# Kernel optimization log

Hardware: AMD Instinct MI355X
Metric: run time of the kernel (lower is better)

## Reference

```python
import jax, jax.numpy as jnp
import numpy as np

HEADS = 4

def _proj(x, w, b):
    # 1x1 conv == per-pixel linear: x [B,C,H,W], w [O,C], b [O]
    return jnp.einsum('oc,bchw->bohw', w, x) + b[None, :, None, None]

def setup_inputs() -> dict:
    key = jax.random.key(0)
    ks = jax.random.split(key, 9)
    B, C, H, W = 16, 512, 32, 32
    emb = C // HEADS
    return {
        'x': jax.random.normal(ks[0], (B, C, H, W), jnp.float32),
        'wq_w': jax.random.normal(ks[1], (C, C), jnp.float32) * 0.02,
        'wq_b': jax.random.normal(ks[2], (C,), jnp.float32) * 0.02,
        'wk_w': jax.random.normal(ks[3], (C, C), jnp.float32) * 0.02,
        'wk_b': jax.random.normal(ks[4], (C,), jnp.float32) * 0.02,
        'wv_w': jax.random.normal(ks[5], (C, C), jnp.float32) * 0.02,
        'wv_b': jax.random.normal(ks[6], (C,), jnp.float32) * 0.02,
        'rh': jax.random.normal(ks[7], (1, HEADS, emb, 1, H), jnp.float32),
        'rw': jax.random.normal(ks[8], (1, HEADS, emb, W, 1), jnp.float32),
    }

def reference(x, wq_w, wq_b, wk_w, wk_b, wv_w, wv_b, rh, rw):
    B, C, H, W = x.shape
    heads = HEADS
    emb = C // heads
    scale = C ** (-0.5)
    N = H * W
    q = _proj(x, wq_w, wq_b).reshape(B, heads, emb, N).transpose(0, 1, 3, 2) * scale  # [B,h,N,d]
    kt = _proj(x, wk_w, wk_b).reshape(B, heads, emb, N)                               # [B,h,d,N]
    v = _proj(x, wv_w, wv_b).reshape(B, heads, emb, N).transpose(0, 1, 3, 2)          # [B,h,N,d]
    qkt = jnp.matmul(q, kt)                                                           # [B,h,N,N]
    # relative-position term: (rh + rw) broadcasts to [1,h,d,W,H], flattened as in source
    rt = (rh + rw).reshape(1, heads, emb, N)
    qrt = jnp.matmul(q, rt)                                                           # [B,h,N,N]
    attn = jax.nn.softmax(qkt + qrt, axis=-1)
    y = jnp.matmul(attn, v)                                                           # [B,h,N,d]
    return y.reshape(B, C, H, W)
```

## Files before the change

### kernel.cpp

```cpp
#include <hip/hip_runtime.h>
#include <hip/hip_bf16.h>
#include <cstdint>

#define NB 16
#define NC 512
#define NPIX 1024
#define NHEADS 4
#define NEMB 128

typedef short bf16x8 __attribute__((ext_vector_type(8)));
typedef float f32x4 __attribute__((ext_vector_type(4)));
typedef float f32x16 __attribute__((ext_vector_type(16)));
typedef unsigned short u16x4 __attribute__((ext_vector_type(4)));
typedef unsigned short u16x8 __attribute__((ext_vector_type(8)));

__device__ __forceinline__ unsigned short f2bf(float f) {
  union { float f; unsigned u; } c; c.f = f;
  return (unsigned short)((c.u + 0x7FFFu + ((c.u >> 16) & 1u)) >> 16);
}

__device__ __forceinline__ unsigned cvtpk_bf16(float lo, float hi) {
  unsigned r;
  asm("v_cvt_pk_bf16_f32 %0, %1, %2" : "=v"(r) : "v"(lo), "v"(hi));
  return r;
}

__device__ __forceinline__ void gload_lds16(const void* g, void* l) {
  __builtin_amdgcn_global_load_lds(
      (const __attribute__((address_space(1))) unsigned int*)g,
      (__attribute__((address_space(3))) unsigned int*)l, 16, 0, 0);
}

__global__ void k_prep_x(const float* __restrict__ x, unsigned short* __restrict__ xt) {
  __shared__ float tile[4][32][33];
  int bid = blockIdx.x;
  int nt = bid & 31, ct4 = (bid >> 5) & 3, b = bid >> 7;
  int n0 = nt * 32, c0 = ct4 * 128;
  int t = threadIdx.x;
  int r = t >> 3, q = t & 7;
#pragma unroll
  for (int s = 0; s < 4; s++) {
    float4 v = *(const float4*)(x + ((size_t)(b * NC + c0 + s * 32 + r)) * NPIX + n0 + q * 4);
    tile[s][r][q * 4 + 0] = v.x; tile[s][r][q * 4 + 1] = v.y;
    tile[s][r][q * 4 + 2] = v.z; tile[s][r][q * 4 + 3] = v.w;
  }
  __syncthreads();
  int cl = q * 4;
#pragma unroll
  for (int s = 0; s < 4; s++) {
    u16x4 o;
    o[0] = f2bf(tile[s][cl + 0][r]); o[1] = f2bf(tile[s][cl + 1][r]);
    o[2] = f2bf(tile[s][cl + 2][r]); o[3] = f2bf(tile[s][cl + 3][r]);
    *(u16x4*)(xt + ((size_t)(b * NPIX + n0 + r)) * NC + c0 + s * 32 + cl) = o;
  }
}

__global__ void k_prep_w(const float* __restrict__ wq, const float* __restrict__ wk,
                         const float* __restrict__ wv, unsigned short* __restrict__ wb) {
  const float* src = blockIdx.y == 0 ? wq : (blockIdx.y == 1 ? wk : wv);
  unsigned short* dst = wb + (size_t)blockIdx.y * NC * NC;
  for (int i = blockIdx.x * 256 + threadIdx.x; i < NC * NC / 4; i += gridDim.x * 256) {
    float4 v = ((const float4*)src)[i];
    u16x4 o = { f2bf(v.x), f2bf(v.y), f2bf(v.z), f2bf(v.w) };
    ((u16x4*)dst)[i] = o;
  }
}

__global__ __launch_bounds__(256, 3) void k_qkv(
    const unsigned short* __restrict__ wb, const unsigned short* __restrict__ xt,
    const float* __restrict__ qb, const float* __restrict__ kb, const float* __restrict__ vb,
    const float* __restrict__ rh, const float* __restrict__ rw,
    unsigned short* __restrict__ Qs, unsigned short* __restrict__ Kn,
    unsigned short* __restrict__ Vm) {
  __shared__ unsigned short Alds[128 * 64];
  __shared__ unsigned short Blds[128 * 64];
  int bid = blockIdx.x;
  int nt = bid & 7, mt = (bid >> 3) & 3;
  int rest = bid >> 5;
  int p = rest % 3, b = rest / 3;
  int m0 = mt * 128, n0 = nt * 128;
  const unsigned short* A = wb + (size_t)p * NC * NC + (size_t)m0 * NC;
  const unsigned short* Bx = xt + (size_t)b * NPIX * NC + (size_t)n0 * NC;
  int t = threadIdx.x;
  int lane = t & 63, wid = t >> 6;
  int wm = (wid >> 1) * 64, wn = (wid & 1) * 64;
  f32x4 acc[4][4] = {};
  for (int k0 = 0; k0 < NC; k0 += 64) {
#pragma unroll
    for (int i = 0; i < 4; i++) {
      int idx = i * 256 + t;
      int row = idx >> 3, col = (idx & 7) * 8;
      gload_lds16(A + (size_t)row * NC + k0 + col, &Alds[idx * 8]);
    }
#pragma unroll
    for (int i = 0; i < 4; i++) {
      int idx = i * 256 + t;
      int row = idx >> 3, col = (idx & 7) * 8;
      gload_lds16(Bx + (size_t)row * NC + k0 + col, &Blds[idx * 8]);
    }
    __syncthreads();
#pragma unroll
    for (int ks = 0; ks < 2; ks++) {
      int kk = ks * 32 + ((lane >> 4) << 3);
      bf16x8 af[4], bfr[4];
#pragma unroll
      for (int f = 0; f < 4; f++)
        af[f] = *(const bf16x8*)&Alds[(wm + f * 16 + (lane & 15)) * 64 + kk];
#pragma unroll
      for (int f = 0; f < 4; f++)
        bfr[f] = *(const bf16x8*)&Blds[(wn + f * 16 + (lane & 15)) * 64 + kk];
#pragma unroll
      for (int fm = 0; fm < 4; fm++)
#pragma unroll
        for (int fn = 0; fn < 4; fn++)
          acc[fm][fn] = __builtin_amdgcn_mfma_f32_16x16x32_bf16(af[fm], bfr[fn], acc[fm][fn], 0, 0, 0);
    }
    __syncthreads();
  }
  const float scale = 0.044194173824159216f * 1.4426950408889634f;
  if (p == 2) {
    char* vbase = (char*)(Vm + (size_t)(b * NHEADS + mt) * 16 * 8192);
#pragma unroll
    for (int fm = 0; fm < 4; fm++) {
#pragma unroll
      for (int r = 0; r < 4; r++) {
        int d = wm + fm * 16 + ((lane >> 4) << 2) + r;
        float bv = vb[m0 + d];
        char* vt = vbase + (size_t)d * 128;
#pragma unroll
        for (int fn = 0; fn < 4; fn++) {
          int j = n0 + wn + fn * 16 + (lane & 15);
          int tile = j >> 6, jl = j & 63;
          *(unsigned short*)(vt + tile * 16384 + (((jl * 2)) ^ ((d & 7) << 4))) =
              f2bf(acc[fm][fn][r] + bv);
        }
      }
    }
  } else if (p == 1) {
    char* kbase = (char*)(Kn + (size_t)(b * NHEADS + mt) * 16 * 8192);
#pragma unroll
    for (int fm = 0; fm < 4; fm++) {
      int e0 = wm + fm * 16 + ((lane >> 4) << 2);
#pragma unroll
      for (int fn = 0; fn < 4; fn++) {
        int j = n0 + wn + fn * 16 + (lane & 15);
        int tile = j >> 6, jl = j & 63;
        u16x4 o;
#pragma unroll
        for (int r = 0; r < 4; r++) {
          float v = acc[fm][fn][r] + kb[m0 + e0 + r];
          v += rh[(m0 + e0 + r) * 32 + (j & 31)] + rw[(m0 + e0 + r) * 32 + (j >> 5)];
          o[r] = f2bf(v);
        }
        *(u16x4*)(kbase + tile * 16384 + jl * 256 + ((2 * e0) ^ ((jl & 7) << 4))) = o;
      }
    }
  } else {
    unsigned short* dst = Qs + ((size_t)((b * NHEADS + mt) * NPIX + n0)) * NEMB;
#pragma unroll
    for (int fm = 0; fm < 4; fm++) {
      int e0 = wm + fm * 16 + ((lane >> 4) << 2);
#pragma unroll
      for (int fn = 0; fn < 4; fn++) {
        int ncol = wn + fn * 16 + (lane & 15);
        u16x4 o;
#pragma unroll
        for (int r = 0; r < 4; r++)
          o[r] = f2bf((acc[fm][fn][r] + qb[m0 + e0 + r]) * scale);
        *(u16x4*)&dst[(size_t)ncol * NEMB + e0] = o;
      }
    }
  }
}

__global__ __launch_bounds__(256, 2) void k_attn(
    const unsigned short* __restrict__ Qs, const unsigned short* __restrict__ Kp,
    const unsigned short* __restrict__ Vp, float* __restrict__ out) {
  __shared__ __align__(16) char smem[65536];
  int bid = blockIdx.x;
  int pair = bid & 63;
  int b = pair >> 2, hd = pair & 3;
  int i0 = (bid >> 6) * 128;
  int t = threadIdx.x, w = t >> 6, lane = t & 63;
  int l31 = lane & 31, hi5 = lane >> 5;
  const unsigned short* Qb = Qs + (size_t)pair * NPIX * NEMB;
  const char* Kpb = (const char*)(Kp + (size_t)pair * 16 * 8192);
  const char* Vpb = (const char*)(Vp + (size_t)pair * 16 * 8192);

  bf16x8 qf[8];
  {
    const unsigned short* qr = Qb + (size_t)(i0 + w * 32 + l31) * NEMB + hi5 * 8;
#pragma unroll
    for (int d8 = 0; d8 < 8; d8++) qf[d8] = *(const bf16x8*)(qr + d8 * 16);
  }
  f32x16 yacc[4] = {};
  float l = 0.f;

#pragma unroll
  for (int r = 0; r < 4; r++) {
    gload_lds16(Kpb + r * 4096 + t * 16, smem + r * 4096 + t * 16);
    gload_lds16(Vpb + r * 4096 + t * 16, smem + 32768 + r * 4096 + t * 16);
  }
  __syncthreads();

  for (int tt = 0; tt < 16; tt++) {
    int cur = tt & 1;
    if (tt < 15) {
      const char* kn = Kpb + (tt + 1) * 16384;
      const char* vn = Vpb + (tt + 1) * 16384;
      char* kd = smem + (cur ^ 1) * 16384;
      char* vd = smem + 32768 + (cur ^ 1) * 16384;
#pragma unroll
      for (int r = 0; r < 4; r++) {
        gload_lds16(kn + r * 4096 + t * 16, kd + r * 4096 + t * 16);
        gload_lds16(vn + r * 4096 + t * 16, vd + r * 4096 + t * 16);
      }
    }
    const char* Kl = smem + cur * 16384;
    const char* Vl = smem + 32768 + cur * 16384;
    f32x16 sacc[2] = {};
    {
      int swz = (l31 & 7) << 4;
#pragma unroll
      for (int d8 = 0; d8 < 8; d8++) {
        int colb = (d8 * 32 + hi5 * 16) ^ swz;
        bf16x8 k0 = *(const bf16x8*)(Kl + l31 * 256 + colb);
        bf16x8 k1 = *(const bf16x8*)(Kl + (32 + l31) * 256 + colb);
        __builtin_amdgcn_s_setprio(1);
        sacc[0] = __builtin_amdgcn_mfma_f32_32x32x16_bf16(k0, qf[d8], sacc[0], 0, 0, 0);
        sacc[1] = __builtin_amdgcn_mfma_f32_32x32x16_bf16(k1, qf[d8], sacc[1], 0, 0, 0);
        __builtin_amdgcn_s_setprio(0);
      }
    }
    float rs0 = 0.f, rs1 = 0.f, rs2 = 0.f, rs3 = 0.f;
#pragma unroll
    for (int c = 0; c < 2; c++)
#pragma unroll
      for (int i = 0; i < 16; i += 4) {
        float p0 = exp2f(sacc[c][i + 0]);
        float p1 = exp2f(sacc[c][i + 1]);
        float p2 = exp2f(sacc[c][i + 2]);
        float p3 = exp2f(sacc[c][i + 3]);
        sacc[c][i + 0] = p0; sacc[c][i + 1] = p1;
        sacc[c][i + 2] = p2; sacc[c][i + 3] = p3;
        rs0 += p0; rs1 += p1; rs2 += p2; rs3 += p3;
      }
    l += (rs0 + rs1) + (rs2 + rs3);
    unsigned up[2][4][2];
#pragma unroll
    for (int c = 0; c < 2; c++)
#pragma unroll
      for (int g = 0; g < 4; g++) {
        up[c][g][0] = cvtpk_bf16(sacc[c][4 * g + 0], sacc[c][4 * g + 1]);
        up[c][g][1] = cvtpk_bf16(sacc[c][4 * g + 2], sacc[c][4 * g + 3]);
      }
    bf16x8 pf[4];
#pragma unroll
    for (int c2 = 0; c2 < 4; c2++) {
      int c = c2 >> 1, gA = (c2 & 1) * 2, gB = gA + 1;
      unsigned a0 = up[c][gA][0], b0 = up[c][gB][0];
      unsigned a1 = up[c][gA][1], b1 = up[c][gB][1];
      asm("v_permlane32_swap_b32 %0, %1" : "+v"(a0), "+v"(b0));
      asm("v_permlane32_swap_b32 %0, %1" : "+v"(a1), "+v"(b1));
      unsigned wd[4] = { a0, a1, b0, b1 };
      pf[c2] = *(bf16x8*)wd;
    }
    {
      int swz = (l31 & 7) << 4;
#pragma unroll
      for (int c2 = 0; c2 < 4; c2++) {
        int colb = (c2 * 32 + hi5 * 16) ^ swz;
        __builtin_amdgcn_s_setprio(1);
#pragma unroll
        for (int ds = 0; ds < 4; ds++) {
          bf16x8 vf = *(const bf16x8*)(Vl + (ds * 32 + l31) * 128 + colb);
          yacc[ds] = __builtin_amdgcn_mfma_f32_32x32x16_bf16(vf, pf[c2], yacc[ds], 0, 0, 0);
        }
        __builtin_amdgcn_s_setprio(0);
      }
    }
    __syncthreads();
  }
  float ltot = l + __shfl_xor(l, 32);
  float invl = 1.0f / ltot;
  int q = i0 + w * 32 + l31;
  float* orow = out + ((size_t)(b * NC + hd * NEMB + (q >> 3))) * NPIX + (q & 7) * NEMB;
#pragma unroll
  for (int ds = 0; ds < 4; ds++)
#pragma unroll
    for (int rg = 0; rg < 4; rg++) {
      f32x4 v;
#pragma unroll
      for (int i = 0; i < 4; i++) v[i] = yacc[ds][rg * 4 + i] * invl;
      *(f32x4*)(orow + ds * 32 + rg * 8 + hi5 * 4) = v;
    }
}

extern "C" void kernel_launch(void* const* d_in, const int* in_sizes, int n_in,
                              void* d_out, int out_size, void* d_ws, size_t ws_size,
                              hipStream_t stream) {
  const float* x  = (const float*)d_in[0];
  const float* wq = (const float*)d_in[1];
  const float* qb = (const float*)d_in[2];
  const float* wk = (const float*)d_in[3];
  const float* kb = (const float*)d_in[4];
  const float* wv = (const float*)d_in[5];
  const float* vb = (const float*)d_in[6];
  const float* rh = (const float*)d_in[7];
  const float* rw = (const float*)d_in[8];
  float* out = (float*)d_out;
  char* ws = (char*)d_ws;
  unsigned short* xt = (unsigned short*)(ws);
  unsigned short* wb = (unsigned short*)(ws + 16777216);
  unsigned short* Q  = (unsigned short*)(ws + 18350080);
  unsigned short* K  = (unsigned short*)(ws + 35127296);
  unsigned short* V  = (unsigned short*)(ws + 51904512);
  k_prep_x<<<2048, 256, 0, stream>>>(x, xt);
  k_prep_w<<<dim3(64, 3), 256, 0, stream>>>(wq, wk, wv, wb);
  k_qkv<<<1536, 256, 0, stream>>>(wb, xt, qb, kb, vb, rh, rw, Q, K, V);
  k_attn<<<512, 256, 0, stream>>>(Q, K, V, out);
}
```

Before: 103.6 us.

## Load K/V fragments directly from global memory in MFMA-ready layout, drop LDS staging

The projection kernel now writes K and V in a fragment-major layout, so each lane's 16-byte MFMA operand sits contiguously in global memory. The attention kernel drops the double-buffered LDS staging and its barriers and reads K/V fragments straight from global (and L2) into registers each tile. This removes LDS traffic and block-wide synchronisation. In exchange, each of the four waves re-reads the same K/V from cache, raising global/L2 load volume, register pressure from holding 32 fragment registers, and exposing load latency without explicit prefetch.

```diff
diff --git a/kernel.cpp b/kernel.cpp
--- a/kernel.cpp
+++ b/kernel.cpp
@@ -119,28 +119,29 @@
   }
   const float scale = 0.044194173824159216f * 1.4426950408889634f;
   if (p == 2) {
-    char* vbase = (char*)(Vm + (size_t)(b * NHEADS + mt) * 16 * 8192);
+    unsigned short* vbase = Vm + (size_t)(b * NHEADS + mt) * 131072;
 #pragma unroll
     for (int fm = 0; fm < 4; fm++) {
 #pragma unroll
       for (int r = 0; r < 4; r++) {
         int d = wm + fm * 16 + ((lane >> 4) << 2) + r;
         float bv = vb[m0 + d];
-        char* vt = vbase + (size_t)d * 128;
 #pragma unroll
         for (int fn = 0; fn < 4; fn++) {
           int j = n0 + wn + fn * 16 + (lane & 15);
           int tile = j >> 6, jl = j & 63;
-          *(unsigned short*)(vt + tile * 16384 + (((jl * 2)) ^ ((d & 7) << 4))) =
-              f2bf(acc[fm][fn][r] + bv);
+          int c2 = jl >> 4, h5 = (jl >> 3) & 1, j8 = jl & 7;
+          size_t flat = ((((size_t)tile * 4 + c2) * 2 + h5) * 128 + d) * 8 + j8;
+          vbase[flat] = f2bf(acc[fm][fn][r] + bv);
         }
       }
     }
   } else if (p == 1) {
-    char* kbase = (char*)(Kn + (size_t)(b * NHEADS + mt) * 16 * 8192);
+    unsigned short* kbase = Kn + (size_t)(b * NHEADS + mt) * 131072;
 #pragma unroll
     for (int fm = 0; fm < 4; fm++) {
       int e0 = wm + fm * 16 + ((lane >> 4) << 2);
+      int d8 = e0 >> 4, h5 = (e0 >> 3) & 1, e8 = e0 & 7;
 #pragma unroll
       for (int fn = 0; fn < 4; fn++) {
         int j = n0 + wn + fn * 16 + (lane & 15);
@@ -152,7 +153,8 @@
           v += rh[(m0 + e0 + r) * 32 + (j & 31)] + rw[(m0 + e0 + r) * 32 + (j >> 5)];
           o[r] = f2bf(v);
         }
-        *(u16x4*)(kbase + tile * 16384 + jl * 256 + ((2 * e0) ^ ((jl & 7) << 4))) = o;
+        size_t flat = ((((size_t)tile * 8 + d8) * 2 + h5) * 64 + jl) * 8 + e8;
+        *(u16x4*)(kbase + flat) = o;
       }
     }
   } else {
@@ -176,7 +178,6 @@
 __global__ __launch_bounds__(256, 2) void k_attn(
     const unsigned short* __restrict__ Qs, const unsigned short* __restrict__ Kp,
     const unsigned short* __restrict__ Vp, float* __restrict__ out) {
-  __shared__ __align__(16) char smem[65536];
   int bid = blockIdx.x;
   int pair = bid & 63;
   int b = pair >> 2, hd = pair & 3;
@@ -184,8 +185,8 @@
   int t = threadIdx.x, w = t >> 6, lane = t & 63;
   int l31 = lane & 31, hi5 = lane >> 5;
   const unsigned short* Qb = Qs + (size_t)pair * NPIX * NEMB;
-  const char* Kpb = (const char*)(Kp + (size_t)pair * 16 * 8192);
-  const char* Vpb = (const char*)(Vp + (size_t)pair * 16 * 8192);
+  const unsigned short* Kg = Kp + (size_t)pair * 131072;
+  const unsigned short* Vg = Vp + (size_t)pair * 131072;
 
   bf16x8 qf[8];
   {
@@ -196,42 +197,29 @@
   f32x16 yacc[4] = {};
   float l = 0.f;
 
-#pragma unroll
-  for (int r = 0; r < 4; r++) {
-    gload_lds16(Kpb + r * 4096 + t * 16, smem + r * 4096 + t * 16);
-    gload_lds16(Vpb + r * 4096 + t * 16, smem + 32768 + r * 4096 + t * 16);
-  }
-  __syncthreads();
-
   for (int tt = 0; tt < 16; tt++) {
-    int cur = tt & 1;
-    if (tt < 15) {
-      const char* kn = Kpb + (tt + 1) * 16384;
-      const char* vn = Vpb + (tt + 1) * 16384;
-      char* kd = smem + (cur ^ 1) * 16384;
-      char* vd = smem + 32768 + (cur ^ 1) * 16384;
-#pragma unroll
-      for (int r = 0; r < 4; r++) {
-        gload_lds16(kn + r * 4096 + t * 16, kd + r * 4096 + t * 16);
-        gload_lds16(vn + r * 4096 + t * 16, vd + r * 4096 + t * 16);
-      }
-    }
-    const char* Kl = smem + cur * 16384;
-    const char* Vl = smem + 32768 + cur * 16384;
+    bf16x8 kf0[8], kf1[8];
+#pragma unroll
+    for (int d8 = 0; d8 < 8; d8++) {
+      const unsigned short* kp = Kg + (((size_t)tt * 8 + d8) * 2 + hi5) * 512;
+      kf0[d8] = *(const bf16x8*)(kp + l31 * 8);
+      kf1[d8] = *(const bf16x8*)(kp + (l31 + 32) * 8);
+    }
     f32x16 sacc[2] = {};
-    {
-      int swz = (l31 & 7) << 4;
-#pragma unroll
-      for (int d8 = 0; d8 < 8; d8++) {
-        int colb = (d8 * 32 + hi5 * 16) ^ swz;
-        bf16x8 k0 = *(const bf16x8*)(Kl + l31 * 256 + colb);
-        bf16x8 k1 = *(const bf16x8*)(Kl + (32 + l31) * 256 + colb);
-        __builtin_amdgcn_s_setprio(1);
-        sacc[0] = __builtin_amdgcn_mfma_f32_32x32x16_bf16(k0, qf[d8], sacc[0], 0, 0, 0);
-        sacc[1] = __builtin_amdgcn_mfma_f32_32x32x16_bf16(k1, qf[d8], sacc[1], 0, 0, 0);
-        __builtin_amdgcn_s_setprio(0);
-      }
-    }
+    __builtin_amdgcn_s_setprio(1);
+#pragma unroll
+    for (int d8 = 0; d8 < 8; d8++) {
+      sacc[0] = __builtin_amdgcn_mfma_f32_32x32x16_bf16(kf0[d8], qf[d8], sacc[0], 0, 0, 0);
+      sacc[1] = __builtin_amdgcn_mfma_f32_32x32x16_bf16(kf1[d8], qf[d8], sacc[1], 0, 0, 0);
+    }
+    __builtin_amdgcn_s_setprio(0);
+    bf16x8 vf[4][4];
+#pragma unroll
+    for (int c2 = 0; c2 < 4; c2++)
+#pragma unroll
+      for (int ds = 0; ds < 4; ds++)
+        vf[c2][ds] = *(const bf16x8*)(
+            Vg + ((((size_t)tt * 4 + c2) * 2 + hi5) * 128 + ds * 32 + l31) * 8);
     float rs0 = 0.f, rs1 = 0.f, rs2 = 0.f, rs3 = 0.f;
 #pragma unroll
     for (int c = 0; c < 2; c++)
@@ -265,21 +253,13 @@
       unsigned wd[4] = { a0, a1, b0, b1 };
       pf[c2] = *(bf16x8*)wd;
     }
-    {
-      int swz = (l31 & 7) << 4;
-#pragma unroll
-      for (int c2 = 0; c2 < 4; c2++) {
-        int colb = (c2 * 32 + hi5 * 16) ^ swz;
-        __builtin_amdgcn_s_setprio(1);
-#pragma unroll
-        for (int ds = 0; ds < 4; ds++) {
-          bf16x8 vf = *(const bf16x8*)(Vl + (ds * 32 + l31) * 128 + colb);
-          yacc[ds] = __builtin_amdgcn_mfma_f32_32x32x16_bf16(vf, pf[c2], yacc[ds], 0, 0, 0);
-        }
-        __builtin_amdgcn_s_setprio(0);
-      }
-    }
-    __syncthreads();
+    __builtin_amdgcn_s_setprio(1);
+#pragma unroll
+    for (int c2 = 0; c2 < 4; c2++)
+#pragma unroll
+      for (int ds = 0; ds < 4; ds++)
+        yacc[ds] = __builtin_amdgcn_mfma_f32_32x32x16_bf16(vf[c2][ds], pf[c2], yacc[ds], 0, 0, 0);
+    __builtin_amdgcn_s_setprio(0);
   }
   float ltot = l + __shfl_xor(l, 32);
   float invl = 1.0f / ltot;
```

Result: slower. 107.6 us (+3.9%).

## Split attention key range across two wave groups per block and merge

Applied to the files above, without the earlier changes.

The attention kernel now launches 512 threads per block. Two halves of the block each process half of every 64-key tile (32 keys) for the same 128 queries, and their partial outputs and row sums are merged through shared memory at the end. The K and V workspace layouts in the projection kernel are changed to 32-key sub-tiles with new swizzles so each half reads its own contiguous region. This aims to raise the number of waves in flight and hide latency. The cost is an extra reduction pass through LDS and a slightly larger shared-memory footprint.

```diff
diff --git a/kernel.cpp b/kernel.cpp
--- a/kernel.cpp
+++ b/kernel.cpp
@@ -119,32 +119,30 @@
   }
   const float scale = 0.044194173824159216f * 1.4426950408889634f;
   if (p == 2) {
-    char* vbase = (char*)(Vm + (size_t)(b * NHEADS + mt) * 16 * 8192);
+    char* vbase = (char*)(Vm + (size_t)(b * NHEADS + mt) * 131072);
 #pragma unroll
     for (int fm = 0; fm < 4; fm++) {
 #pragma unroll
       for (int r = 0; r < 4; r++) {
         int d = wm + fm * 16 + ((lane >> 4) << 2) + r;
         float bv = vb[m0 + d];
-        char* vt = vbase + (size_t)d * 128;
 #pragma unroll
         for (int fn = 0; fn < 4; fn++) {
           int j = n0 + wn + fn * 16 + (lane & 15);
-          int tile = j >> 6, jl = j & 63;
-          *(unsigned short*)(vt + tile * 16384 + (((jl * 2)) ^ ((d & 7) << 4))) =
+          *(unsigned short*)(vbase + (size_t)(j >> 5) * 8192 + d * 64 +
+                             (((j & 31) * 2) ^ ((d & 3) << 4))) =
               f2bf(acc[fm][fn][r] + bv);
         }
       }
     }
   } else if (p == 1) {
-    char* kbase = (char*)(Kn + (size_t)(b * NHEADS + mt) * 16 * 8192);
+    char* kbase = (char*)(Kn + (size_t)(b * NHEADS + mt) * 131072);
 #pragma unroll
     for (int fm = 0; fm < 4; fm++) {
       int e0 = wm + fm * 16 + ((lane >> 4) << 2);
 #pragma unroll
       for (int fn = 0; fn < 4; fn++) {
         int j = n0 + wn + fn * 16 + (lane & 15);
-        int tile = j >> 6, jl = j & 63;
         u16x4 o;
 #pragma unroll
         for (int r = 0; r < 4; r++) {
@@ -152,7 +150,7 @@
           v += rh[(m0 + e0 + r) * 32 + (j & 31)] + rw[(m0 + e0 + r) * 32 + (j >> 5)];
           o[r] = f2bf(v);
         }
-        *(u16x4*)(kbase + tile * 16384 + jl * 256 + ((2 * e0) ^ ((jl & 7) << 4))) = o;
+        *(u16x4*)(kbase + (size_t)j * 256 + ((2 * e0) ^ ((j & 15) << 4))) = o;
       }
     }
   } else {
@@ -173,127 +171,136 @@
   }
 }
 
-__global__ __launch_bounds__(256, 2) void k_attn(
+__global__ __launch_bounds__(512, 4) void k_attn(
     const unsigned short* __restrict__ Qs, const unsigned short* __restrict__ Kp,
     const unsigned short* __restrict__ Vp, float* __restrict__ out) {
-  __shared__ __align__(16) char smem[65536];
+  __shared__ __align__(16) char smem[68096];
   int bid = blockIdx.x;
   int pair = bid & 63;
   int b = pair >> 2, hd = pair & 3;
   int i0 = (bid >> 6) * 128;
   int t = threadIdx.x, w = t >> 6, lane = t & 63;
   int l31 = lane & 31, hi5 = lane >> 5;
+  int h = w >> 2, wq = w & 3;
   const unsigned short* Qb = Qs + (size_t)pair * NPIX * NEMB;
-  const char* Kpb = (const char*)(Kp + (size_t)pair * 16 * 8192);
-  const char* Vpb = (const char*)(Vp + (size_t)pair * 16 * 8192);
+  const char* Kpb = (const char*)(Kp + (size_t)pair * 131072);
+  const char* Vpb = (const char*)(Vp + (size_t)pair * 131072);
 
   bf16x8 qf[8];
   {
-    const unsigned short* qr = Qb + (size_t)(i0 + w * 32 + l31) * NEMB + hi5 * 8;
+    const unsigned short* qr = Qb + (size_t)(i0 + wq * 32 + l31) * NEMB + hi5 * 8;
 #pragma unroll
     for (int d8 = 0; d8 < 8; d8++) qf[d8] = *(const bf16x8*)(qr + d8 * 16);
   }
   f32x16 yacc[4] = {};
   float l = 0.f;
 
-#pragma unroll
-  for (int r = 0; r < 4; r++) {
-    gload_lds16(Kpb + r * 4096 + t * 16, smem + r * 4096 + t * 16);
-    gload_lds16(Vpb + r * 4096 + t * 16, smem + 32768 + r * 4096 + t * 16);
-  }
+  auto stage = [&](int tile, int slot) {
+    char* kd = smem + slot * 16384;
+    char* vd = smem + 32768 + slot * 16384;
+#pragma unroll
+    for (int ii = 0; ii < 2; ii++) {
+      const char* ks = Kpb + (size_t)((ii * 16 + tile) * 8192) + t * 16;
+      const char* vs = Vpb + (size_t)((ii * 16 + tile) * 8192) + t * 16;
+      gload_lds16(ks, kd + (ii * 512 + t) * 16);
+      gload_lds16(vs, vd + (ii * 512 + t) * 16);
+    }
+  };
+
+  stage(0, 0);
   __syncthreads();
+
+  const int kswz = (l31 & 15) << 4;
+  const int vswz = (l31 & 3) << 4;
 
   for (int tt = 0; tt < 16; tt++) {
     int cur = tt & 1;
-    if (tt < 15) {
-      const char* kn = Kpb + (tt + 1) * 16384;
-      const char* vn = Vpb + (tt + 1) * 16384;
-      char* kd = smem + (cur ^ 1) * 16384;
-      char* vd = smem + 32768 + (cur ^ 1) * 16384;
-#pragma unroll
-      for (int r = 0; r < 4; r++) {
-        gload_lds16(kn + r * 4096 + t * 16, kd + r * 4096 + t * 16);
-        gload_lds16(vn + r * 4096 + t * 16, vd + r * 4096 + t * 16);
-      }
-    }
-    const char* Kl = smem + cur * 16384;
-    const char* Vl = smem + 32768 + cur * 16384;
-    f32x16 sacc[2] = {};
+    if (tt < 15) stage(tt + 1, cur ^ 1);
+    const char* Kl = smem + cur * 16384 + h * 8192;
+    const char* Vl = smem + 32768 + cur * 16384 + h * 8192;
+    f32x16 sacc = (f32x16)(0.0f);
+    __builtin_amdgcn_s_setprio(1);
+#pragma unroll
+    for (int d8 = 0; d8 < 8; d8++) {
+      bf16x8 k0 = *(const bf16x8*)(Kl + l31 * 256 + ((d8 * 32 + hi5 * 16) ^ kswz));
+      sacc = __builtin_amdgcn_mfma_f32_32x32x16_bf16(k0, qf[d8], sacc, 0, 0, 0);
+    }
+    __builtin_amdgcn_s_setprio(0);
+    float rs0, rs1, rs2, rs3;
     {
-      int swz = (l31 & 7) << 4;
-#pragma unroll
-      for (int d8 = 0; d8 < 8; d8++) {
-        int colb = (d8 * 32 + hi5 * 16) ^ swz;
-        bf16x8 k0 = *(const bf16x8*)(Kl + l31 * 256 + colb);
-        bf16x8 k1 = *(const bf16x8*)(Kl + (32 + l31) * 256 + colb);
-        __builtin_amdgcn_s_setprio(1);
-        sacc[0] = __builtin_amdgcn_mfma_f32_32x32x16_bf16(k0, qf[d8], sacc[0], 0, 0, 0);
-        sacc[1] = __builtin_amdgcn_mfma_f32_32x32x16_bf16(k1, qf[d8], sacc[1], 0, 0, 0);
-        __builtin_amdgcn_s_setprio(0);
-      }
-    }
-    float rs0 = 0.f, rs1 = 0.f, rs2 = 0.f, rs3 = 0.f;
-#pragma unroll
-    for (int c = 0; c < 2; c++)
-#pragma unroll
-      for (int i = 0; i < 16; i += 4) {
-        float p0 = exp2f(sacc[c][i + 0]);
-        float p1 = exp2f(sacc[c][i + 1]);
-        float p2 = exp2f(sacc[c][i + 2]);
-        float p3 = exp2f(sacc[c][i + 3]);
-        sacc[c][i + 0] = p0; sacc[c][i + 1] = p1;
-        sacc[c][i + 2] = p2; sacc[c][i + 3] = p3;
-        rs0 += p0; rs1 += p1; rs2 += p2; rs3 += p3;
-      }
+      float p0 = exp2f(sacc[0]), p1 = exp2f(sacc[1]), p2 = exp2f(sacc[2]), p3 = exp2f(sacc[3]);
+      sacc[0] = p0; sacc[1] = p1; sacc[2] = p2; sacc[3] = p3;
+      rs0 = p0; rs1 = p1; rs2 = p2; rs3 = p3;
+    }
+#pragma unroll
+    for (int i = 4; i < 16; i += 4) {
+      float p0 = exp2f(sacc[i + 0]);
+      float p1 = exp2f(sacc[i + 1]);
+      float p2 = exp2f(sacc[i + 2]);
+      float p3 = exp2f(sacc[i + 3]);
+      sacc[i + 0] = p0; sacc[i + 1] = p1; sacc[i + 2] = p2; sacc[i + 3] = p3;
+      rs0 += p0; rs1 += p1; rs2 += p2; rs3 += p3;
+    }
     l += (rs0 + rs1) + (rs2 + rs3);
-    unsigned up[2][4][2];
-#pragma unroll
-    for (int c = 0; c < 2; c++)
-#pragma unroll
-      for (int g = 0; g < 4; g++) {
-        up[c][g][0] = cvtpk_bf16(sacc[c][4 * g + 0], sacc[c][4 * g + 1]);
-        up[c][g][1] = cvtpk_bf16(sacc[c][4 * g + 2], sacc[c][4 * g + 3]);
-      }
-    bf16x8 pf[4];
-#pragma unroll
-    for (int c2 = 0; c2 < 4; c2++) {
-      int c = c2 >> 1, gA = (c2 & 1) * 2, gB = gA + 1;
-      unsigned a0 = up[c][gA][0], b0 = up[c][gB][0];
-      unsigned a1 = up[c][gA][1], b1 = up[c][gB][1];
+    unsigned up[4][2];
+#pragma unroll
+    for (int g = 0; g < 4; g++) {
+      up[g][0] = cvtpk_bf16(sacc[4 * g + 0], sacc[4 * g + 1]);
+      up[g][1] = cvtpk_bf16(sacc[4 * g + 2], sacc[4 * g + 3]);
+    }
+#pragma unroll
+    for (int c2 = 0; c2 < 2; c2++) {
+      int gA = c2 * 2, gB = gA + 1;
+      unsigned a0 = up[gA][0], b0 = up[gB][0];
+      unsigned a1 = up[gA][1], b1 = up[gB][1];
       asm("v_permlane32_swap_b32 %0, %1" : "+v"(a0), "+v"(b0));
       asm("v_permlane32_swap_b32 %0, %1" : "+v"(a1), "+v"(b1));
       unsigned wd[4] = { a0, a1, b0, b1 };
-      pf[c2] = *(bf16x8*)wd;
-    }
-    {
-      int swz = (l31 & 7) << 4;
-#pragma unroll
-      for (int c2 = 0; c2 < 4; c2++) {
-        int colb = (c2 * 32 + hi5 * 16) ^ swz;
-        __builtin_amdgcn_s_setprio(1);
-#pragma unroll
-        for (int ds = 0; ds < 4; ds++) {
-          bf16x8 vf = *(const bf16x8*)(Vl + (ds * 32 + l31) * 128 + colb);
-          yacc[ds] = __builtin_amdgcn_mfma_f32_32x32x16_bf16(vf, pf[c2], yacc[ds], 0, 0, 0);
-        }
-        __builtin_amdgcn_s_setprio(0);
-      }
+      bf16x8 pf = *(bf16x8*)wd;
+      __builtin_amdgcn_s_setprio(1);
+#pragma unroll
+      for (int ds = 0; ds < 4; ds++) {
+        bf16x8 vf = *(const bf16x8*)(
+            Vl + (ds * 32 + l31) * 64 + ((c2 * 32 + hi5 * 16) ^ vswz));
+        yacc[ds] = __builtin_amdgcn_mfma_f32_32x32x16_bf16(vf, pf, yacc[ds], 0, 0, 0);
+      }
+      __builtin_amdgcn_s_setprio(0);
     }
     __syncthreads();
   }
-  float ltot = l + __shfl_xor(l, 32);
-  float invl = 1.0f / ltot;
-  int q = i0 + w * 32 + l31;
-  float* orow = out + ((size_t)(b * NC + hd * NEMB + (q >> 3))) * NPIX + (q & 7) * NEMB;
-#pragma unroll
-  for (int ds = 0; ds < 4; ds++)
-#pragma unroll
-    for (int rg = 0; rg < 4; rg++) {
-      f32x4 v;
-#pragma unroll
-      for (int i = 0; i < 4; i++) v[i] = yacc[ds][rg * 4 + i] * invl;
-      *(f32x4*)(orow + ds * 32 + rg * 8 + hi5 * 4) = v;
-    }
+
+  float l_own = l + __shfl_xor(l, 32);
+  float* ex = (float*)smem;
+  float* Lw = (float*)(smem + 67584);
+  int q = wq * 32 + l31;
+  if (h == 1) {
+#pragma unroll
+    for (int ds = 0; ds < 4; ds++)
+#pragma unroll
+      for (int rg = 0; rg < 4; rg++) {
+        f32x4 v;
+#pragma unroll
+        for (int i = 0; i < 4; i++) v[i] = yacc[ds][rg * 4 + i];
+        *(f32x4*)(ex + q * 132 + ds * 32 + rg * 8 + hi5 * 4) = v;
+      }
+    if (hi5 == 0) Lw[q] = l_own;
+  }
+  __syncthreads();
+  if (h == 0) {
+    float invl = 1.0f / (l_own + Lw[q]);
+    int qg = i0 + q;
+    float* orow = out + ((size_t)(b * NC + hd * NEMB + (qg >> 3))) * NPIX + (qg & 7) * NEMB;
+#pragma unroll
+    for (int ds = 0; ds < 4; ds++)
+#pragma unroll
+      for (int rg = 0; rg < 4; rg++) {
+        f32x4 v2 = *(const f32x4*)(ex + q * 132 + ds * 32 + rg * 8 + hi5 * 4);
+        f32x4 v;
+#pragma unroll
+        for (int i = 0; i < 4; i++) v[i] = (yacc[ds][rg * 4 + i] + v2[i]) * invl;
+        *(f32x4*)(orow + ds * 32 + rg * 8 + hi5 * 4) = v;
+      }
+  }
 }
 
 extern "C" void kernel_launch(void* const* d_in, const int* in_sizes, int n_in,
@@ -318,5 +325,5 @@
   k_prep_x<<<2048, 256, 0, stream>>>(x, xt);
   k_prep_w<<<dim3(64, 3), 256, 0, stream>>>(wq, wk, wv, wb);
   k_qkv<<<1536, 256, 0, stream>>>(wb, xt, qb, kb, vb, rh, rw, Q, K, V);
-  k_attn<<<512, 256, 0, stream>>>(Q, K, V, out);
-}
+  k_attn<<<512, 512, 0, stream>>>(Q, K, V, out);
+}
```

Result: slower. 118.9 us (+14.8%).
